# Kernel tuning notes

Hardware: AMD Instinct MI355X
Metric: run time of the kernel (lower is better)

Reference implementation:

```python
import jax, jax.numpy as jnp
import numpy as np

TAU = 2.0
GAMMA = 1.0 - 1.0 / TAU
V_TH = 1.0

# Rectangle surrogate: heaviside forward, rectangular window gradient (|x| < 0.5)
@jax.custom_vjp
def rect_spike(x):
    return (x >= 0.0).astype(x.dtype)

def _rect_fwd(x):
    return rect_spike(x), x

def _rect_bwd(x, g):
    return (g * (jnp.abs(x) < 0.5).astype(g.dtype),)

rect_spike.defvjp(_rect_fwd, _rect_bwd)


def setup_inputs() -> dict:
    key = jax.random.key(0)
    x_seq = jax.random.normal(key, (64, 128, 4096), dtype=jnp.float32)  # [T, B, D]
    return {"x_seq": x_seq}


def reference(x_seq) -> jnp.ndarray:
    # CLIF recurrence over timestep axis 0. Note: in the original torch code,
    # torch.sigmoid_(m) is in-place, so m is replaced by sigmoid(m) after the
    # reset line; we reproduce that exactly.
    gamma = jnp.asarray(GAMMA, x_seq.dtype)
    one_minus_gamma = jnp.asarray(1.0 - GAMMA, x_seq.dtype)
    zero = jnp.zeros(x_seq.shape[1:], x_seq.dtype)

    def step(carry, x_t):
        u, m = carry
        u = gamma * u + x_t
        spike = rect_spike(u - V_TH)
        m = m * jax.nn.sigmoid(one_minus_gamma * u) + spike
        sm = jax.nn.sigmoid(m)          # in-place sigmoid_: m becomes sigmoid(m)
        u = u - spike * (V_TH + sm)
        return (u, sm), spike

    _, spikes = jax.lax.scan(step, (zero, zero), x_seq)
    return spikes  # [T, B, D]
```

## Files before the change

### kernel.cpp

```cpp
#include <hip/hip_runtime.h>
#include <math.h>


#define T_STEPS 64
#define BD      (128 * 4096)
#define N4      (BD / 4)

__device__ __forceinline__ float sigmoid_cr(float x) {
    const double SHIFT = 6755399441055744.0;
    double xd = (double)x;
    double t  = xd * -1.4426950408889634;
    double tn = t + SHIFT;
    int    n  = __double2loint(tn);
    double f  = t - (tn - SHIFT);
    double y  = f * 0.6931471805599453;
    double p = 2.755731922398589e-7;
    p = fma(p, y, 2.755731922398589e-6);
    p = fma(p, y, 2.480158730158730e-5);
    p = fma(p, y, 1.984126984126984e-4);
    p = fma(p, y, 1.388888888888889e-3);
    p = fma(p, y, 8.333333333333333e-3);
    p = fma(p, y, 4.166666666666666e-2);
    p = fma(p, y, 1.666666666666667e-1);
    p = fma(p, y, 0.5);
    p = fma(p, y, 1.0);
    p = fma(p, y, 1.0);
    double sc = __hiloint2double(0x3FF00000 + ((unsigned)n << 20), 0);
    double e  = p * sc;
    double d  = 1.0 + e;
    double r = (double)__builtin_amdgcn_rcpf((float)d);
    r = r * fma(-d, r, 2.0);
    r = r * fma(-d, r, 2.0);
    return (float)r;
}

__device__ __forceinline__ float clif_step(float& u, float& m, float x) {
    u = __fadd_rn(__fmul_rn(0.5f, u), x);
    float spike = (u >= 1.0f) ? 1.0f : 0.0f;
    float s1 = sigmoid_cr(__fmul_rn(0.5f, u));
    float mn = __fadd_rn(__fmul_rn(m, s1), spike);
    float sm = sigmoid_cr(mn);
    u = __fsub_rn(u, __fmul_rn(spike, __fadd_rn(1.0f, sm)));
    m = sm;
    return spike;
}

__global__ __launch_bounds__(256) void clif_kernel(const float4* __restrict__ x4,
                                                   float4* __restrict__ o4) {
    int gid = blockIdx.x * blockDim.x + threadIdx.x;

    float u0 = 0.f, u1 = 0.f, u2 = 0.f, u3 = 0.f;
    float m0 = 0.f, m1 = 0.f, m2 = 0.f, m3 = 0.f;

    float4 xv = x4[gid];
    #pragma unroll 1
    for (int t = 0; t < T_STEPS; ++t) {
        float4 xn;
        if (t + 1 < T_STEPS)
            xn = x4[(size_t)(t + 1) * N4 + gid];
        float4 sp;
        sp.x = clif_step(u0, m0, xv.x);
        sp.y = clif_step(u1, m1, xv.y);
        sp.z = clif_step(u2, m2, xv.z);
        sp.w = clif_step(u3, m3, xv.w);
        o4[(size_t)t * N4 + gid] = sp;
        xv = xn;
    }
}

extern "C" void kernel_launch(void* const* d_in, const int* in_sizes, int n_in,
                              void* d_out, int out_size, void* d_ws, size_t ws_size,
                              hipStream_t stream) {
    const float4* x = (const float4*)d_in[0];
    float4* out = (float4*)d_out;
    dim3 block(256);
    dim3 grid(N4 / 256);
    clif_kernel<<<grid, block, 0, stream>>>(x, out);
}
```

Measured before the change: 75.16 us.

## Use one element per thread with scalar loads and drop a Newton refinement step

Each thread now handles one element instead of four, so the grid is four times larger and the accesses become scalar instead of float4. The launch bound asks for eight blocks per CU so more waves can hide the long serial double-precision sigmoid chain. The second Newton-Raphson step in the reciprocal is also removed, which cuts double-precision FMAs. The trade-offs are narrower memory transactions, the loss of ILP across four independent elements per thread, and a reciprocal that may no longer round correctly in rare cases.

```diff
diff --git a/kernel.cpp b/kernel.cpp
--- a/kernel.cpp
+++ b/kernel.cpp
@@ -4,12 +4,10 @@
 
 #define T_STEPS 64
 #define BD      (128 * 4096)
-#define N4      (BD / 4)
 
 __device__ __forceinline__ float sigmoid_cr(float x) {
     const double SHIFT = 6755399441055744.0;
-    double xd = (double)x;
-    double t  = xd * -1.4426950408889634;
+    double t  = (double)x * -1.4426950408889634;
     double tn = t + SHIFT;
     int    n  = __double2loint(tn);
     double f  = t - (tn - SHIFT);
@@ -30,7 +28,6 @@
     double d  = 1.0 + e;
     double r = (double)__builtin_amdgcn_rcpf((float)d);
     r = r * fma(-d, r, 2.0);
-    r = r * fma(-d, r, 2.0);
     return (float)r;
 }
 
@@ -45,25 +42,19 @@
     return spike;
 }
 
-__global__ __launch_bounds__(256) void clif_kernel(const float4* __restrict__ x4,
-                                                   float4* __restrict__ o4) {
+__global__ __launch_bounds__(256, 8) void clif_kernel(const float* __restrict__ x,
+                                                      float* __restrict__ o) {
     int gid = blockIdx.x * blockDim.x + threadIdx.x;
 
-    float u0 = 0.f, u1 = 0.f, u2 = 0.f, u3 = 0.f;
-    float m0 = 0.f, m1 = 0.f, m2 = 0.f, m3 = 0.f;
-
-    float4 xv = x4[gid];
+    float u = 0.f, m = 0.f;
+    float xv = x[gid];
     #pragma unroll 1
     for (int t = 0; t < T_STEPS; ++t) {
-        float4 xn;
+        float xn;
         if (t + 1 < T_STEPS)
-            xn = x4[(size_t)(t + 1) * N4 + gid];
-        float4 sp;
-        sp.x = clif_step(u0, m0, xv.x);
-        sp.y = clif_step(u1, m1, xv.y);
-        sp.z = clif_step(u2, m2, xv.z);
-        sp.w = clif_step(u3, m3, xv.w);
-        o4[(size_t)t * N4 + gid] = sp;
+            xn = x[(size_t)(t + 1) * BD + gid];
+        float sp = clif_step(u, m, xv);
+        o[(size_t)t * BD + gid] = sp;
         xv = xn;
     }
 }
@@ -71,9 +62,9 @@
 extern "C" void kernel_launch(void* const* d_in, const int* in_sizes, int n_in,
                               void* d_out, int out_size, void* d_ws, size_t ws_size,
                               hipStream_t stream) {
-    const float4* x = (const float4*)d_in[0];
-    float4* out = (float4*)d_out;
+    const float* x = (const float*)d_in[0];
+    float* out = (float*)d_out;
     dim3 block(256);
-    dim3 grid(N4 / 256);
+    dim3 grid(BD / 256);
     clif_kernel<<<grid, block, 0, stream>>>(x, out);
 }
```

Measured after the change: 70.64 us. 1.06x faster.
